# Optimization experiments

Measured on AMD Instinct MI355X. Metric: run time of the kernel, lower is better.

## Reference

```python
import jax, jax.numpy as jnp
import numpy as np

D_MODEL = 1024
NUM_HEADS = 16
HEAD_DIM = D_MODEL // NUM_HEADS
BATCH, SEQ = 2, 2048


def setup_inputs() -> dict:
    key = jax.random.key(0)
    ks = jax.random.split(key, 5)
    scale = 1.0 / np.sqrt(D_MODEL)  # ~xavier magnitude
    x = jax.random.normal(ks[0], (BATCH, SEQ, D_MODEL), dtype=jnp.float32)
    Wq = jax.random.normal(ks[1], (D_MODEL, D_MODEL), dtype=jnp.float32) * scale
    Wk = jax.random.normal(ks[2], (D_MODEL, D_MODEL), dtype=jnp.float32) * scale
    Wv = jax.random.normal(ks[3], (D_MODEL, D_MODEL), dtype=jnp.float32) * scale
    Wo = jax.random.normal(ks[4], (D_MODEL, D_MODEL), dtype=jnp.float32) * scale
    z = jnp.zeros((D_MODEL,), dtype=jnp.float32)
    return {"x": x, "Wq": Wq, "bq": z, "Wk": Wk, "bk": z, "Wv": Wv, "bv": z, "Wo": Wo, "bo": z}


def reference(x, Wq, bq, Wk, bk, Wv, bv, Wo, bo):
    B, S, _ = x.shape
    H, Dh = NUM_HEADS, HEAD_DIM
    # torch Linear convention: y = x @ W^T + b
    q = (x @ Wq.T + bq).reshape(B, S, H, Dh)
    k = (x @ Wk.T + bk).reshape(B, S, H, Dh)
    v = (x @ Wv.T + bv).reshape(B, S, H, Dh)
    # scores: [B, H, S, S]
    scores = jnp.einsum('bqhd,bkhd->bhqk', q, k) / np.sqrt(Dh).astype(np.float32)
    attn = jax.nn.softmax(scores, axis=-1)
    out = jnp.einsum('bhqk,bkhd->bqhd', attn, v).reshape(B, S, H * Dh)
    return out @ Wo.T + bo
```

## Files before the change

kernel.cpp:

```cpp
#include <hip/hip_runtime.h>
#include <hip/hip_bf16.h>

typedef __bf16 bf16;
typedef __bf16 bf16x8 __attribute__((ext_vector_type(8)));
typedef __bf16 bf16x4 __attribute__((ext_vector_type(4)));
typedef float f32x4 __attribute__((ext_vector_type(4)));

constexpr int DM = 1024, NH = 16, DH = 64, NB = 2, SQ = 2048;
constexpr int MTOT = NB * SQ;
constexpr float QSCALE = 0.125f * 1.44269504088896f;

__device__ __forceinline__ void gld_lds16(const bf16* g, bf16* l) {
  __builtin_amdgcn_global_load_lds(
      (const __attribute__((address_space(1))) void*)g,
      (__attribute__((address_space(3))) void*)l, 16, 0, 0);
}

__global__ __launch_bounds__(256) void cvt5(
    const float* __restrict__ s0, const float* __restrict__ s1,
    const float* __restrict__ s2, const float* __restrict__ s3,
    const float* __restrict__ s4,
    bf16* __restrict__ d0, bf16* __restrict__ d1, bf16* __restrict__ d2,
    bf16* __restrict__ d3, bf16* __restrict__ d4) {
  const float* src; bf16* dst; int n;
  switch (blockIdx.y) {
    case 0: src = s0; dst = d0; n = DM * DM; break;
    case 1: src = s1; dst = d1; n = DM * DM; break;
    case 2: src = s2; dst = d2; n = DM * DM; break;
    case 3: src = s3; dst = d3; n = DM * DM; break;
    default: src = s4; dst = d4; n = MTOT * DM; break;
  }
  const int idx = (blockIdx.x * 256 + threadIdx.x) * 4;
  if (idx < n) {
    const float4 v = *(const float4*)(src + idx);
    *(bf16x4*)(dst + idx) = (bf16x4){(bf16)v.x, (bf16)v.y, (bf16)v.z, (bf16)v.w};
  }
}

template <typename OutT>
__device__ __forceinline__ void gemm_tile(
    const bf16* __restrict__ A, const bf16* __restrict__ Bm,
    const float* __restrict__ bias, OutT* __restrict__ C,
    int rowA0, int rowB0, int N, int K, bool bias_row, float cscale,
    bf16* sA, bf16* sB) {
  const int tid = threadIdx.x;
  const int wave = tid >> 6, lane = tid & 63;
  const int wm = wave >> 1, wn = wave & 1;
  const int quad = lane >> 4, l16 = lane & 15;

  f32x4 acc[4][4];
#pragma unroll
  for (int i = 0; i < 4; i++)
#pragma unroll
    for (int j = 0; j < 4; j++) acc[i][j] = (f32x4){0.f, 0.f, 0.f, 0.f};

  const int srow = lane >> 3;
  const int scol = ((lane & 7) ^ srow) * 8;

  for (int kt = 0; kt < K; kt += 64) {
#pragma unroll
    for (int i = 0; i < 4; i++) {
      const int r = (wave * 4 + i) * 8;
      gld_lds16(A + (size_t)(rowA0 + r + srow) * K + kt + scol, &sA[r * 64]);
      gld_lds16(Bm + (size_t)(rowB0 + r + srow) * K + kt + scol, &sB[r * 64]);
    }
    __syncthreads();
#pragma unroll
    for (int kk = 0; kk < 64; kk += 32) {
      bf16x8 aF[4], bF[4];
      const int slot = (((kk >> 3) + quad) ^ (l16 & 7)) << 3;
#pragma unroll
      for (int mt = 0; mt < 4; mt++)
        aF[mt] = *(const bf16x8*)&sA[(wm * 64 + mt * 16 + l16) * 64 + slot];
#pragma unroll
      for (int nt = 0; nt < 4; nt++)
        bF[nt] = *(const bf16x8*)&sB[(wn * 64 + nt * 16 + l16) * 64 + slot];
#pragma unroll
      for (int mt = 0; mt < 4; mt++)
#pragma unroll
        for (int nt = 0; nt < 4; nt++)
          acc[mt][nt] = __builtin_amdgcn_mfma_f32_16x16x32_bf16(aF[mt], bF[nt], acc[mt][nt], 0, 0, 0);
    }
    __syncthreads();
  }

#pragma unroll
  for (int mt = 0; mt < 4; mt++) {
#pragma unroll
    for (int nt = 0; nt < 4; nt++) {
#pragma unroll
      for (int r = 0; r < 4; r++) {
        const int row = rowA0 + wm * 64 + mt * 16 + quad * 4 + r;
        const int col = rowB0 + wn * 64 + nt * 16 + l16;
        const float bb = bias_row ? bias[row] : bias[col];
        C[(size_t)row * N + col] = (OutT)((acc[mt][nt][r] + bb) * cscale);
      }
    }
  }
}

__global__ __launch_bounds__(256, 2) void qkv_gemm(
    const bf16* __restrict__ xb, const bf16* __restrict__ Wqb,
    const bf16* __restrict__ Wkb, const bf16* __restrict__ Wvb,
    const float* __restrict__ bq, const float* __restrict__ bk,
    const float* __restrict__ bv,
    bf16* __restrict__ Qw, bf16* __restrict__ Kw, bf16* __restrict__ VTw) {
  __shared__ alignas(16) bf16 sA[128 * 64];
  __shared__ alignas(16) bf16 sB[128 * 64];
  if (blockIdx.z == 0) {
    gemm_tile<bf16>(xb, Wqb, bq, Qw, blockIdx.x * 128, blockIdx.y * 128, DM, DM, false, QSCALE, sA, sB);
  } else if (blockIdx.z == 1) {
    gemm_tile<bf16>(xb, Wkb, bk, Kw, blockIdx.x * 128, blockIdx.y * 128, DM, DM, false, 1.0f, sA, sB);
  } else {
    const int id = blockIdx.y * 32 + blockIdx.x;
    gemm_tile<bf16>(Wvb, xb, bv, VTw, (id >> 5) * 128, (id & 31) * 128, MTOT, DM, true, 1.0f, sA, sB);
  }
}

__global__ __launch_bounds__(256, 2) void out_gemm(
    const bf16* __restrict__ A, const bf16* __restrict__ Bm,
    const float* __restrict__ bias, float* __restrict__ C) {
  __shared__ alignas(16) bf16 sA[128 * 64];
  __shared__ alignas(16) bf16 sB[128 * 64];
  gemm_tile<float>(A, Bm, bias, C, blockIdx.x * 128, blockIdx.y * 128, DM, DM, false, 1.0f, sA, sB);
}

__global__ __launch_bounds__(256, 3) void attn(
    const bf16* __restrict__ Q, const bf16* __restrict__ Kq,
    const bf16* __restrict__ VT, bf16* __restrict__ O) {
  __shared__ alignas(16) bf16 sK[128 * 64];
  __shared__ alignas(16) bf16 sV[64 * 128];
  __shared__ alignas(16) bf16 sP[4][32 * 64];
  const int tid = threadIdx.x, wave = tid >> 6, lane = tid & 63;
  const int quad = lane >> 4, l16 = lane & 15;
  const int hb = blockIdx.x, qt = blockIdx.y;
  const int h = hb & 15, b = hb >> 4;

  const bf16* Qg = Q + (size_t)(b * SQ + qt * 128) * DM + h * DH;
  const bf16* Kg = Kq + (size_t)(b * SQ) * DM + h * DH;
  const bf16* Vg = VT + (size_t)(h * DH) * MTOT + b * SQ;

  const int srow = lane >> 3, scol = ((lane & 7) ^ srow) * 8;
  const int vrow = lane >> 4;

  bf16x8 qF[2][2];
#pragma unroll
  for (int mt = 0; mt < 2; mt++)
#pragma unroll
    for (int kkh = 0; kkh < 2; kkh++)
      qF[mt][kkh] = *(const bf16x8*)(Qg + (size_t)(wave * 32 + mt * 16 + l16) * DM +
                                     kkh * 32 + quad * 8);

  float l_i[2] = {0.f, 0.f};
  f32x4 o_acc[2][4];
#pragma unroll
  for (int mt = 0; mt < 2; mt++)
#pragma unroll
    for (int n2 = 0; n2 < 4; n2++) o_acc[mt][n2] = (f32x4){0.f, 0.f, 0.f, 0.f};

  for (int t = 0; t < 16; ++t) {
#pragma unroll
    for (int i = 0; i < 4; i++) {
      const int r = (wave * 4 + i) * 8;
      gld_lds16(Kg + (size_t)(t * 128 + r + srow) * DM + scol, &sK[r * 64]);
    }
#pragma unroll
    for (int i = 0; i < 4; i++) {
      const int r = (wave * 4 + i) * 4;
      const int vchunk = (lane & 15) ^ ((r + vrow) & 7);
      gld_lds16(Vg + (size_t)(r + vrow) * MTOT + t * 128 + vchunk * 8, &sV[r * 128]);
    }
    __syncthreads();

    f32x4 sacc[2][8];
#pragma unroll
    for (int mt = 0; mt < 2; mt++)
#pragma unroll
      for (int nt = 0; nt < 8; nt++) sacc[mt][nt] = (f32x4){0.f, 0.f, 0.f, 0.f};
#pragma unroll
    for (int kk = 0; kk < 64; kk += 32) {
      bf16x8 kF[8];
      const int slot = (((kk >> 3) + quad) ^ (l16 & 7)) << 3;
#pragma unroll
      for (int nt = 0; nt < 8; nt++)
        kF[nt] = *(const bf16x8*)&sK[(nt * 16 + l16) * 64 + slot];
#pragma unroll
      for (int mt = 0; mt < 2; mt++)
#pragma unroll
        for (int nt = 0; nt < 8; nt++)
          sacc[mt][nt] = __builtin_amdgcn_mfma_f32_16x16x32_bf16(kF[nt], qF[mt][kk >> 5],
                                                                 sacc[mt][nt], 0, 0, 0);
    }

#pragma unroll
    for (int half = 0; half < 2; half++) {
#pragma unroll
      for (int mt = 0; mt < 2; mt++) {
        const int row = mt * 16 + l16;
#pragma unroll
        for (int nt4 = 0; nt4 < 4; nt4++) {
          const f32x4 s = sacc[mt][half * 4 + nt4];
          bf16x4 pk;
#pragma unroll
          for (int r = 0; r < 4; r++) {
            const float p = __builtin_amdgcn_exp2f(s[r]);
            l_i[mt] += p;
            pk[r] = (bf16)p;
          }
          const int c = 2 * nt4 + (quad >> 1);
          *(bf16x4*)&sP[wave][row * 64 + ((c ^ (row & 7)) << 3) + (quad & 1) * 4] = pk;
        }
      }
#pragma unroll
      for (int kk = 0; kk < 64; kk += 32) {
        bf16x8 pF[2], vF[4];
#pragma unroll
        for (int mt = 0; mt < 2; mt++) {
          const int row = mt * 16 + l16;
          const int c = (kk >> 3) + quad;
          pF[mt] = *(const bf16x8*)&sP[wave][row * 64 + ((c ^ (row & 7)) << 3)];
        }
#pragma unroll
        for (int n2 = 0; n2 < 4; n2++) {
          const int ch = ((half * 64 + kk) >> 3) + quad;
          vF[n2] = *(const bf16x8*)&sV[(n2 * 16 + l16) * 128 + ((ch ^ (l16 & 7)) << 3)];
        }
#pragma unroll
        for (int mt = 0; mt < 2; mt++)
#pragma unroll
          for (int n2 = 0; n2 < 4; n2++)
            o_acc[mt][n2] = __builtin_amdgcn_mfma_f32_16x16x32_bf16(pF[mt], vF[n2],
                                                                    o_acc[mt][n2], 0, 0, 0);
      }
    }
    __syncthreads();
  }

  float* lbuf = (float*)&sP[wave][0];
#pragma unroll
  for (int mt = 0; mt < 2; mt++) {
    float v = l_i[mt];
    v += __shfl_xor(v, 16);
    v += __shfl_xor(v, 32);
    if (quad == 0) lbuf[mt * 16 + l16] = v;
  }
  __builtin_amdgcn_s_waitcnt(0);
#pragma unroll
  for (int mt = 0; mt < 2; mt++) {
    const f32x4 lv = *(const f32x4*)&lbuf[mt * 16 + quad * 4];
#pragma unroll
    for (int r = 0; r < 4; r++) {
      const float inv = 1.0f / lv[r];
      const int row = qt * 128 + wave * 32 + mt * 16 + quad * 4 + r;
#pragma unroll
      for (int n2 = 0; n2 < 4; n2++) {
        const int col = n2 * 16 + l16;
        O[(size_t)(b * SQ + row) * DM + h * DH + col] = (bf16)(o_acc[mt][n2][r] * inv);
      }
    }
  }
}

extern "C" void kernel_launch(void* const* d_in, const int* in_sizes, int n_in,
                              void* d_out, int out_size, void* d_ws, size_t ws_size,
                              hipStream_t stream) {
  const float* x  = (const float*)d_in[0];
  const float* Wq = (const float*)d_in[1];
  const float* bq = (const float*)d_in[2];
  const float* Wk = (const float*)d_in[3];
  const float* bk = (const float*)d_in[4];
  const float* Wv = (const float*)d_in[5];
  const float* bv = (const float*)d_in[6];
  const float* Wo = (const float*)d_in[7];
  const float* bo = (const float*)d_in[8];
  float* out = (float*)d_out;

  bf16* ws   = (bf16*)d_ws;
  bf16* xb   = ws;
  bf16* Wqb  = ws + (size_t)MTOT * DM;
  bf16* Wkb  = Wqb + (size_t)DM * DM;
  bf16* Wvb  = Wkb + (size_t)DM * DM;
  bf16* Wob  = Wvb + (size_t)DM * DM;
  bf16* Qw   = Wob + (size_t)DM * DM;
  bf16* Kw   = Qw + (size_t)MTOT * DM;
  bf16* VTw  = Kw + (size_t)MTOT * DM;
  bf16* Cw   = VTw + (size_t)MTOT * DM;

  const dim3 blk(256);
  cvt5<<<dim3(MTOT * DM / 1024, 5), blk, 0, stream>>>(Wq, Wk, Wv, Wo, x,
                                                      Wqb, Wkb, Wvb, Wob, xb);
  qkv_gemm<<<dim3(32, 8, 3), blk, 0, stream>>>(xb, Wqb, Wkb, Wvb, bq, bk, bv, Qw, Kw, VTw);
  attn<<<dim3(NH * NB, SQ / 128), blk, 0, stream>>>(Qw, Kw, VTw, Cw);
  out_gemm<<<dim3(MTOT / 128, DM / 128), blk, 0, stream>>>(Cw, Wob, bo, out);
}
```

Before: 192.2 us.

## Double-buffer LDS tiles in GEMM and attention kernels to overlap loads

Both the GEMM tile loop and the attention K/V loop now use two LDS buffers. The next tile's global-to-LDS load is issued right after the barrier and overlaps with MFMA work on the current tile, and the trailing barrier is dropped. This aims to hide global memory latency. In exchange LDS per block doubles, and attention launch bounds drop from 3 to 2 blocks per CU, which lowers occupancy.

```diff
diff --git a/kernel.cpp b/kernel.cpp
--- a/kernel.cpp
+++ b/kernel.cpp
@@ -57,31 +57,38 @@
   const int srow = lane >> 3;
   const int scol = ((lane & 7) ^ srow) * 8;
 
-  for (int kt = 0; kt < K; kt += 64) {
+  auto stage = [&](int kt, int buf) {
 #pragma unroll
     for (int i = 0; i < 4; i++) {
       const int r = (wave * 4 + i) * 8;
-      gld_lds16(A + (size_t)(rowA0 + r + srow) * K + kt + scol, &sA[r * 64]);
-      gld_lds16(Bm + (size_t)(rowB0 + r + srow) * K + kt + scol, &sB[r * 64]);
-    }
+      gld_lds16(A + (size_t)(rowA0 + r + srow) * K + kt + scol, &sA[buf * 8192 + r * 64]);
+      gld_lds16(Bm + (size_t)(rowB0 + r + srow) * K + kt + scol, &sB[buf * 8192 + r * 64]);
+    }
+  };
+
+  stage(0, 0);
+  const int NIT = K / 64;
+  for (int it = 0; it < NIT; it++) {
     __syncthreads();
+    if (it + 1 < NIT) stage((it + 1) * 64, (it + 1) & 1);
+    const bf16* cA = &sA[(it & 1) * 8192];
+    const bf16* cB = &sB[(it & 1) * 8192];
 #pragma unroll
     for (int kk = 0; kk < 64; kk += 32) {
       bf16x8 aF[4], bF[4];
       const int slot = (((kk >> 3) + quad) ^ (l16 & 7)) << 3;
 #pragma unroll
       for (int mt = 0; mt < 4; mt++)
-        aF[mt] = *(const bf16x8*)&sA[(wm * 64 + mt * 16 + l16) * 64 + slot];
+        aF[mt] = *(const bf16x8*)&cA[(wm * 64 + mt * 16 + l16) * 64 + slot];
 #pragma unroll
       for (int nt = 0; nt < 4; nt++)
-        bF[nt] = *(const bf16x8*)&sB[(wn * 64 + nt * 16 + l16) * 64 + slot];
+        bF[nt] = *(const bf16x8*)&cB[(wn * 64 + nt * 16 + l16) * 64 + slot];
 #pragma unroll
       for (int mt = 0; mt < 4; mt++)
 #pragma unroll
         for (int nt = 0; nt < 4; nt++)
           acc[mt][nt] = __builtin_amdgcn_mfma_f32_16x16x32_bf16(aF[mt], bF[nt], acc[mt][nt], 0, 0, 0);
     }
-    __syncthreads();
   }
 
 #pragma unroll
@@ -105,8 +112,8 @@
     const float* __restrict__ bq, const float* __restrict__ bk,
     const float* __restrict__ bv,
     bf16* __restrict__ Qw, bf16* __restrict__ Kw, bf16* __restrict__ VTw) {
-  __shared__ alignas(16) bf16 sA[128 * 64];
-  __shared__ alignas(16) bf16 sB[128 * 64];
+  __shared__ alignas(16) bf16 sA[2 * 128 * 64];
+  __shared__ alignas(16) bf16 sB[2 * 128 * 64];
   if (blockIdx.z == 0) {
     gemm_tile<bf16>(xb, Wqb, bq, Qw, blockIdx.x * 128, blockIdx.y * 128, DM, DM, false, QSCALE, sA, sB);
   } else if (blockIdx.z == 1) {
@@ -120,16 +127,16 @@
 __global__ __launch_bounds__(256, 2) void out_gemm(
     const bf16* __restrict__ A, const bf16* __restrict__ Bm,
     const float* __restrict__ bias, float* __restrict__ C) {
-  __shared__ alignas(16) bf16 sA[128 * 64];
-  __shared__ alignas(16) bf16 sB[128 * 64];
+  __shared__ alignas(16) bf16 sA[2 * 128 * 64];
+  __shared__ alignas(16) bf16 sB[2 * 128 * 64];
   gemm_tile<float>(A, Bm, bias, C, blockIdx.x * 128, blockIdx.y * 128, DM, DM, false, 1.0f, sA, sB);
 }
 
-__global__ __launch_bounds__(256, 3) void attn(
+__global__ __launch_bounds__(256, 2) void attn(
     const bf16* __restrict__ Q, const bf16* __restrict__ Kq,
     const bf16* __restrict__ VT, bf16* __restrict__ O) {
-  __shared__ alignas(16) bf16 sK[128 * 64];
-  __shared__ alignas(16) bf16 sV[64 * 128];
+  __shared__ alignas(16) bf16 sK[2][128 * 64];
+  __shared__ alignas(16) bf16 sV[2][64 * 128];
   __shared__ alignas(16) bf16 sP[4][32 * 64];
   const int tid = threadIdx.x, wave = tid >> 6, lane = tid & 63;
   const int quad = lane >> 4, l16 = lane & 15;
@@ -143,6 +150,20 @@
   const int srow = lane >> 3, scol = ((lane & 7) ^ srow) * 8;
   const int vrow = lane >> 4;
 
+  auto stageKV = [&](int t, int buf) {
+#pragma unroll
+    for (int i = 0; i < 4; i++) {
+      const int r = (wave * 4 + i) * 8;
+      gld_lds16(Kg + (size_t)(t * 128 + r + srow) * DM + scol, &sK[buf][r * 64]);
+    }
+#pragma unroll
+    for (int i = 0; i < 4; i++) {
+      const int r = (wave * 4 + i) * 4;
+      const int vchunk = (lane & 15) ^ ((r + vrow) & 7);
+      gld_lds16(Vg + (size_t)(r + vrow) * MTOT + t * 128 + vchunk * 8, &sV[buf][r * 128]);
+    }
+  };
+
   bf16x8 qF[2][2];
 #pragma unroll
   for (int mt = 0; mt < 2; mt++)
@@ -158,19 +179,12 @@
 #pragma unroll
     for (int n2 = 0; n2 < 4; n2++) o_acc[mt][n2] = (f32x4){0.f, 0.f, 0.f, 0.f};
 
+  stageKV(0, 0);
   for (int t = 0; t < 16; ++t) {
-#pragma unroll
-    for (int i = 0; i < 4; i++) {
-      const int r = (wave * 4 + i) * 8;
-      gld_lds16(Kg + (size_t)(t * 128 + r + srow) * DM + scol, &sK[r * 64]);
-    }
-#pragma unroll
-    for (int i = 0; i < 4; i++) {
-      const int r = (wave * 4 + i) * 4;
-      const int vchunk = (lane & 15) ^ ((r + vrow) & 7);
-      gld_lds16(Vg + (size_t)(r + vrow) * MTOT + t * 128 + vchunk * 8, &sV[r * 128]);
-    }
     __syncthreads();
+    if (t + 1 < 16) stageKV(t + 1, (t + 1) & 1);
+    const bf16* cK = sK[t & 1];
+    const bf16* cV = sV[t & 1];
 
     f32x4 sacc[2][8];
 #pragma unroll
@@ -183,7 +197,7 @@
       const int slot = (((kk >> 3) + quad) ^ (l16 & 7)) << 3;
 #pragma unroll
       for (int nt = 0; nt < 8; nt++)
-        kF[nt] = *(const bf16x8*)&sK[(nt * 16 + l16) * 64 + slot];
+        kF[nt] = *(const bf16x8*)&cK[(nt * 16 + l16) * 64 + slot];
 #pragma unroll
       for (int mt = 0; mt < 2; mt++)
 #pragma unroll
@@ -223,7 +237,7 @@
 #pragma unroll
         for (int n2 = 0; n2 < 4; n2++) {
           const int ch = ((half * 64 + kk) >> 3) + quad;
-          vF[n2] = *(const bf16x8*)&sV[(n2 * 16 + l16) * 128 + ((ch ^ (l16 & 7)) << 3)];
+          vF[n2] = *(const bf16x8*)&cV[(n2 * 16 + l16) * 128 + ((ch ^ (l16 & 7)) << 3)];
         }
 #pragma unroll
         for (int mt = 0; mt < 2; mt++)
@@ -233,7 +247,6 @@
                                                                     o_acc[mt][n2], 0, 0, 0);
       }
     }
-    __syncthreads();
   }
 
   float* lbuf = (float*)&sP[wave][0];
```

Result: no change. 191.1 us (-0.6%).
